# Kernel tuning notes

Hardware: AMD Instinct MI355X
Metric: run time of the kernel (lower is better)

## Reference

```python
import jax, jax.numpy as jnp
import numpy as np

N, E, E_LG, H, KGE, NUM_GRAPHS, N_ITER = 100000, 500000, 1000000, 128, 128, 1024, 2
EPS = 1e-5

def _prelu(x, a):
    return jnp.where(x >= 0, x, a * x)

def _seg_mean(vals, idx, num):
    s = jax.ops.segment_sum(vals, idx, num_segments=num)
    c = jax.ops.segment_sum(jnp.ones((vals.shape[0],), vals.dtype), idx, num_segments=num)
    return s / jnp.maximum(c, 1.0)[:, None]

def setup_inputs() -> dict:
    key = jax.random.key(0)
    ks = jax.random.split(key, 16)
    sc = 1.0 / np.sqrt(H)
    inp = {
        "x": jax.random.normal(ks[0], (N, H), jnp.float32),
        "edge_attr": jax.random.normal(ks[1], (E, H), jnp.float32),
        "edge_index": jax.random.randint(ks[2], (2, E), 0, N),
        "batch": jnp.sort(jax.random.randint(ks[3], (N,), 0, NUM_GRAPHS)),
        "line_graph_edge_index": jax.random.randint(ks[4], (2, E_LG), 0, E),
        # edge_update_net: Linear + PReLU + BatchNorm1d (eval mode)
        "W1": jax.random.normal(ks[5], (H, H), jnp.float32) * sc,
        "b1": jnp.zeros((H,), jnp.float32),
        "a1": jnp.full((1,), 0.25, jnp.float32),
        "bn_gamma": jnp.ones((H,), jnp.float32),
        "bn_beta": jnp.zeros((H,), jnp.float32),
        "bn_mean": jnp.zeros((H,), jnp.float32),
        "bn_var": jnp.ones((H,), jnp.float32),
        # GRU (single layer, single step)
        "w_ih": jax.random.normal(ks[6], (3 * H, H), jnp.float32) * sc,
        "w_hh": jax.random.normal(ks[7], (3 * H, H), jnp.float32) * sc,
        "b_ih": jnp.zeros((3 * H,), jnp.float32),
        "b_hh": jnp.zeros((3 * H,), jnp.float32),
        # DynamicAttention net
        "Wa1": jax.random.normal(ks[8], (H // 2, H), jnp.float32) * sc,
        "ba1": jnp.zeros((H // 2,), jnp.float32),
        "a2": jnp.full((1,), 0.25, jnp.float32),
        "Wa2": jax.random.normal(ks[9], (1, H // 2), jnp.float32) * (1.0 / np.sqrt(H // 2)),
        "ba2": jnp.zeros((1,), jnp.float32),
        # readout
        "Wr": jax.random.normal(ks[10], (KGE, H), jnp.float32) * sc,
        "br": jnp.zeros((KGE,), jnp.float32),
    }
    return inp

def reference(x, edge_attr, W1, b1, a1, bn_gamma, bn_beta, bn_mean, bn_var,
              w_ih, w_hh, b_ih, b_hh, Wa1, ba1, a2, Wa2, ba2, Wr, br,
              edge_index, batch, line_graph_edge_index):
    src, dst = edge_index[0], edge_index[1]
    l_src, l_dst = line_graph_edge_index[0], line_graph_edge_index[1]
    h = x  # GRU hidden state [N, H]
    for _ in range(N_ITER):
        # edge-to-edge message passing (node_to_edge_proj is Identity here)
        fused = edge_attr + (x[src] + x[dst]) * 0.5  # [E, H]
        agg = _seg_mean(fused[l_src], l_dst, E)      # scatter-mean over line graph
        upd = _prelu(agg @ W1.T + b1, a1)
        upd = (upd - bn_mean) * jax.lax.rsqrt(bn_var + EPS) * bn_gamma + bn_beta
        fused = fused + upd
        node_updates = _seg_mean(fused, dst, N)      # [N, H]
        # single GRU step
        gi = node_updates @ w_ih.T + b_ih
        gh = h @ w_hh.T + b_hh
        gi_r, gi_z, gi_n = jnp.split(gi, 3, axis=-1)
        gh_r, gh_z, gh_n = jnp.split(gh, 3, axis=-1)
        r = jax.nn.sigmoid(gi_r + gh_r)
        z = jax.nn.sigmoid(gi_z + gh_z)
        n = jnp.tanh(gi_n + r * gh_n)
        h = (1.0 - z) * n + z * h
        x = h
    # dynamic attention: per-graph scalar gate
    graph_repr = _seg_mean(x, batch, NUM_GRAPHS)     # [G, H]
    attn = jax.nn.sigmoid(_prelu(graph_repr @ Wa1.T + ba1, a2) @ Wa2.T + ba2)  # [G, 1]
    attended = x * attn[batch]
    graph_emb = jax.ops.segment_sum(attended, batch, num_segments=NUM_GRAPHS)
    graph_emb = graph_emb @ Wr.T + br
    return (x, graph_emb)
```

## Files before the change

### kernel.cpp

```cpp
#include <hip/hip_runtime.h>
#include <stdint.h>

#define H 128
#define G_NUM 1024
#define BN_EPS 1e-5f
#define IDXCAP 512

typedef unsigned int uint;
typedef unsigned short ushort;
typedef unsigned char uchar;
typedef __attribute__((ext_vector_type(8))) __bf16 bf16x8;
typedef __attribute__((ext_vector_type(8))) ushort ushort8;
typedef __attribute__((ext_vector_type(4))) float f32x4;
typedef __attribute__((ext_vector_type(2))) float f32x2;

__device__ __forceinline__ float b2f(ushort u){ return __uint_as_float(((uint)u) << 16); }
__device__ __forceinline__ ushort f2b(float f){
    uint u = __float_as_uint(f);
    u += 0x7FFFu + ((u >> 16) & 1u);
    return (ushort)(u >> 16);
}
__device__ __forceinline__ float ldf(const void* p, size_t i, int bf){
    return bf ? b2f(((const ushort*)p)[i]) : ((const float*)p)[i];
}
__device__ __forceinline__ int swz(int r, int byte_in_row){
    return (r * 256 + byte_in_row) ^ ((r & 7) << 4);
}

#define GBODY(SRC, sA, sB) do{ \
    uint4 wA_ = *(const uint4*)((SRC) + (size_t)(sA) * H + ch16 * 8); \
    uint4 wB_ = *(const uint4*)((SRC) + (size_t)(sB) * H + ch16 * 8); \
    uint wa_[4] = {wA_.x, wA_.y, wA_.z, wA_.w}; \
    uint wb_[4] = {wB_.x, wB_.y, wB_.z, wB_.w}; \
    _Pragma("unroll") \
    for (int k2 = 0; k2 < 4; k2++){ \
        f32x2 va_, vb_; \
        va_.x = __uint_as_float(wa_[k2] << 16); va_.y = __uint_as_float(wa_[k2] & 0xFFFF0000u); \
        vb_.x = __uint_as_float(wb_[k2] << 16); vb_.y = __uint_as_float(wb_[k2] & 0xFFFF0000u); \
        accA[k2] += va_; accB[k2] += vb_; \
    } }while(0)

__global__ void k_setup_small(const uint* __restrict__ gamma_bits,
                              const void* b1, const void* a1, const void* gam, const void* bet,
                              const void* mean, const void* var, const void* bih, const void* bhh,
                              float* __restrict__ ep, float* __restrict__ bi, float* __restrict__ bh,
                              int* __restrict__ flag, ushort* __restrict__ fz1, ushort* __restrict__ fz2,
                              size_t zoff, int* __restrict__ lg_off, int E, int ELG,
                              int* __restrict__ nd_off, int N, int Etot){
    __shared__ int bfs;
    int t = threadIdx.x;
    if (t == 0){
        int f = (gamma_bits[0] == 0x3F803F80u) ? 1 : 0;
        *flag = f; bfs = f;
        lg_off[E] = ELG;
        nd_off[N] = Etot;
    }
    __syncthreads();
    int bf = bfs;
    bi[t] = ldf(bih, t, bf);
    bh[t] = ldf(bhh, t, bf);
    if (t < 128){
        ep[t]       = ldf(b1, t, bf);
        ep[128 + t] = rsqrtf(ldf(var, t, bf) + BN_EPS) * ldf(gam, t, bf);
        ep[256 + t] = ldf(mean, t, bf);
        ep[384 + t] = ldf(bet, t, bf);
        fz1[zoff + t] = 0; fz2[zoff + t] = 0;
    }
    if (t == 0) ep[512] = ldf(a1, 0, bf);
}

__global__ __launch_bounds__(256) void k_count_nd(const int* __restrict__ ei, int* __restrict__ cnt, int E){
    int t = blockIdx.x * 256 + threadIdx.x;
    if (t < E) atomicAdd(&cnt[ei[E + t]], 1);
}
__global__ __launch_bounds__(256) void k_fill_nd(const int* __restrict__ ei, const int* __restrict__ off,
                                                 int* __restrict__ cur, int* __restrict__ list, int E){
    int t = blockIdx.x * 256 + threadIdx.x;
    if (t >= E) return;
    int k = ei[E + t];
    int pos = atomicAdd(&cur[k], 1);
    list[off[k] + pos] = t;
}
__global__ __launch_bounds__(256) void k_rank(const int* __restrict__ nd_list, int* __restrict__ rank,
                                              int2* __restrict__ eis, int* __restrict__ e_orig,
                                              const int* __restrict__ ei, int E){
    int j = blockIdx.x * 256 + threadIdx.x;
    if (j >= E) return;
    int e = nd_list[j];
    rank[e] = j;
    eis[j] = make_int2(ei[e], ei[E + e]);
    e_orig[j] = e;
}
__global__ __launch_bounds__(256) void k_count_lg(const int* __restrict__ lgi, const int* __restrict__ rank,
                                                  int* __restrict__ cnt, int ELG){
    int t = blockIdx.x * 256 + threadIdx.x;
    if (t < ELG) atomicAdd(&cnt[rank[lgi[ELG + t]]], 1);
}
__global__ __launch_bounds__(256) void k_fill_lg(const int* __restrict__ lgi, const int* __restrict__ rank,
                                                 const int* __restrict__ off, int* __restrict__ cur,
                                                 int* __restrict__ list, int ELG){
    int t = blockIdx.x * 256 + threadIdx.x;
    if (t >= ELG) return;
    int k = rank[lgi[ELG + t]];
    int pos = atomicAdd(&cur[k], 1);
    list[off[k] + pos] = rank[lgi[t]];
}
__global__ __launch_bounds__(256) void k_scan_reduce(const int* __restrict__ cnt, int* __restrict__ bsum, int n){
    int base = blockIdx.x * 1024;
    int s = 0;
    for (int i = threadIdx.x; i < 1024; i += 256){ int idx = base + i; s += (idx < n) ? cnt[idx] : 0; }
    __shared__ int r[256];
    r[threadIdx.x] = s; __syncthreads();
    for (int o = 128; o > 0; o >>= 1){ if (threadIdx.x < o) r[threadIdx.x] += r[threadIdx.x + o]; __syncthreads(); }
    if (threadIdx.x == 0) bsum[blockIdx.x] = r[0];
}
__global__ __launch_bounds__(256) void k_scan_mid(int* __restrict__ bsum, int nb){
    __shared__ int ts[256];
    int tid = threadIdx.x;
    int loc[4]; int s = 0;
    #pragma unroll
    for (int j = 0; j < 4; j++){
        int idx = tid * 4 + j;
        loc[j] = s;
        s += (idx < nb) ? bsum[idx] : 0;
    }
    ts[tid] = s; __syncthreads();
    for (int o = 1; o < 256; o <<= 1){
        int v = (tid >= o) ? ts[tid - o] : 0;
        __syncthreads();
        ts[tid] += v;
        __syncthreads();
    }
    int texcl = ts[tid] - s;
    #pragma unroll
    for (int j = 0; j < 4; j++){
        int idx = tid * 4 + j;
        if (idx < nb) bsum[idx] = texcl + loc[j];
    }
}
__global__ __launch_bounds__(256) void k_scan_final(const int* __restrict__ cnt, const int* __restrict__ bsum,
                                                    int* __restrict__ off, int n){
    __shared__ int ts[256];
    int base = blockIdx.x * 1024;
    int tid = threadIdx.x;
    int loc[4]; int s = 0;
    #pragma unroll
    for (int j = 0; j < 4; j++){
        int idx = base + tid * 4 + j;
        loc[j] = s;
        s += (idx < n) ? cnt[idx] : 0;
    }
    ts[tid] = s; __syncthreads();
    for (int o = 1; o < 256; o <<= 1){
        int v = (tid >= o) ? ts[tid - o] : 0;
        __syncthreads();
        ts[tid] += v;
        __syncthreads();
    }
    int texcl = ts[tid] - s + bsum[blockIdx.x];
    #pragma unroll
    for (int j = 0; j < 4; j++){
        int idx = base + tid * 4 + j;
        if (idx < n) off[idx] = texcl + loc[j];
    }
}
__global__ __launch_bounds__(256) void k_sortperm(const int* __restrict__ off, uchar* __restrict__ perm, int NK){
    int t = blockIdx.x * 256 + threadIdx.x;
    int wave = t >> 6;
    int l = t & 63;
    int l5 = l & 31;
    int r0 = wave * 32;
    if (r0 >= NK) return;
    int r = r0 + l5;
    int deg = off[r + 1] - off[r];
    int key = (deg << 5) | l5;
    #pragma unroll
    for (int k = 2; k <= 32; k <<= 1){
        #pragma unroll
        for (int j = k >> 1; j > 0; j >>= 1){
            int other = __shfl_xor(key, j);
            bool dir = ((l5 & k) == 0);
            bool lower = ((l5 & j) == 0);
            int mn = min(key, other), mx = max(key, other);
            key = (dir == lower) ? mn : mx;
        }
    }
    if (l < 32) perm[r0 + l5] = (uchar)(key & 31);
}
__global__ __launch_bounds__(256) void k_cvt_bf(const void* __restrict__ in, ushort* __restrict__ out,
                                                int n, const int* __restrict__ flag){
    int t = blockIdx.x * 256 + threadIdx.x;
    if (t >= n) return;
    if (*flag) out[t] = ((const ushort*)in)[t];
    else       out[t] = f2b(((const float*)in)[t]);
}
__global__ __launch_bounds__(256) void k_wcvt(const void* __restrict__ W1, const void* __restrict__ wih,
                                              const void* __restrict__ whh, const void* __restrict__ Wr,
                                              ushort* __restrict__ W1bf, ushort* __restrict__ wihbf,
                                              ushort* __restrict__ whhbf, float* __restrict__ WrT,
                                              const int* __restrict__ flag){
    int t = blockIdx.x * 256 + threadIdx.x;
    int bf = *flag;
    if (t < 16384) W1bf[t] = bf ? ((const ushort*)W1)[t] : f2b(((const float*)W1)[t]);
    else if (t < 65536){ int i = t - 16384; wihbf[i] = bf ? ((const ushort*)wih)[i] : f2b(((const float*)wih)[i]); }
    else if (t < 114688){ int i = t - 65536; whhbf[i] = bf ? ((const ushort*)whh)[i] : f2b(((const float*)whh)[i]); }
    else if (t < 131072){ int i = t - 114688; int r = i >> 7, c = i & 127; WrT[c * 128 + r] = ldf(Wr, i, bf); }
}

__global__ __launch_bounds__(256) void k_fused(const void* __restrict__ ea, const ushort* __restrict__ hb,
                                               const int2* __restrict__ eis, const int* __restrict__ e_orig,
                                               ushort* __restrict__ fused, int E, const int* __restrict__ flag){
    int t = blockIdx.x * 256 + threadIdx.x;
    if (t >= E * 16) return;
    int bf = *flag;
    int j = t >> 4, ch = (t & 15) * 8;
    int2 sd = eis[j];
    int e = e_orig[j];
    size_t src = (size_t)e * H + ch;
    ushort8 hs = *(const ushort8*)(hb + (size_t)sd.x * H + ch);
    ushort8 hd = *(const ushort8*)(hb + (size_t)sd.y * H + ch);
    float av[8];
    if (bf){
        ushort8 a = *(const ushort8*)((const ushort*)ea + src);
        #pragma unroll
        for (int k = 0; k < 8; k++) av[k] = b2f(a[k]);
    } else {
        float4 a0 = *(const float4*)((const float*)ea + src);
        float4 a1 = *(const float4*)((const float*)ea + src + 4);
        av[0] = a0.x; av[1] = a0.y; av[2] = a0.z; av[3] = a0.w;
        av[4] = a1.x; av[5] = a1.y; av[6] = a1.z; av[7] = a1.w;
    }
    ushort8 o;
    #pragma unroll
    for (int k = 0; k < 8; k++) o[k] = f2b(av[k] + 0.5f * (b2f(hs[k]) + b2f(hd[k])));
    *(ushort8*)(fused + (size_t)j * H + ch) = o;
}

__global__ __launch_bounds__(256) void k_agg_gemm(const ushort* __restrict__ fused,
                                                  const int* __restrict__ lg_off, const int* __restrict__ list,
                                                  const uchar* __restrict__ perm,
                                                  const ushort* __restrict__ W1bf, const float* __restrict__ ep,
                                                  ushort* __restrict__ fused2, int E, int LMAX){
    __shared__ __attribute__((aligned(16))) char As[32 * 256];
    __shared__ int idxL[IDXCAP];
    __shared__ int offL[33];
    int tid = threadIdx.x, wid = tid >> 6, lane = tid & 63;
    int r0 = blockIdx.x * 32;
    if (tid < 33) offL[tid] = lg_off[r0 + tid];
    __syncthreads();
    int seg_s = offL[0], seglen = offL[32] - seg_s;
    bool staged = (seglen <= IDXCAP);
    if (staged){ for (int j = tid; j < seglen; j += 256) idxL[j] = list[seg_s + j]; }
    __syncthreads();
    int l16 = lane >> 4, ch16 = lane & 15;
    int rA = wid * 8 + l16, rB = rA + 4;
    int plA = perm[r0 + rA], plB = perm[r0 + rB];
    int baseA = offL[plA], degA = offL[plA + 1] - baseA;
    int baseB = offL[plB], degB = offL[plB + 1] - baseB;
    int dm = max(degA, degB);
    #pragma unroll
    for (int o = 32; o > 0; o >>= 1) dm = max(dm, __shfl_xor(dm, o));
    f32x2 accA[4] = {}, accB[4] = {};
    if (staged){
        int relA = baseA - seg_s, relB = baseB - seg_s;
        #pragma unroll 2
        for (int i = 0; i < dm; i++){
            int liA = min(relA + i, seglen - 1);
            int liB = min(relB + i, seglen - 1);
            int sA = idxL[liA];
            int sB = idxL[liB];
            sA = (i < degA) ? sA : E;
            sB = (i < degB) ? sB : E;
            GBODY(fused, sA, sB);
        }
    } else {
        #pragma unroll 2
        for (int i = 0; i < dm; i++){
            int liA = baseA + i; liA = (liA < LMAX) ? liA : (LMAX - 1);
            int liB = baseB + i; liB = (liB < LMAX) ? liB : (LMAX - 1);
            int sA = list[liA];
            int sB = list[liB];
            sA = (i < degA) ? sA : E;
            sB = (i < degB) ? sB : E;
            GBODY(fused, sA, sB);
        }
    }
    float invA = 1.f / fmaxf((float)degA, 1.f);
    float invB = 1.f / fmaxf((float)degB, 1.f);
    ushort8 oA, oB;
    #pragma unroll
    for (int k2 = 0; k2 < 4; k2++){
        oA[2 * k2] = f2b(accA[k2].x * invA); oA[2 * k2 + 1] = f2b(accA[k2].y * invA);
        oB[2 * k2] = f2b(accB[k2].x * invB); oB[2 * k2 + 1] = f2b(accB[k2].y * invB);
    }
    *(ushort8*)(As + swz(plA, ch16 * 16)) = oA;
    *(ushort8*)(As + swz(plB, ch16 * 16)) = oB;
    __syncthreads();
    int lrow = lane & 15, lhi = lane >> 4;
    f32x4 acc[2][2] = {};
    #pragma unroll
    for (int ks = 0; ks < 4; ks++){
        bf16x8 afr[2];
        #pragma unroll
        for (int rt = 0; rt < 2; rt++)
            afr[rt] = *(const bf16x8*)(As + swz(rt * 16 + lrow, ks * 64 + lhi * 16));
        #pragma unroll
        for (int cc = 0; cc < 2; cc++){
            int c = (2 * wid + cc) * 16 + lrow;
            bf16x8 bfr = *(const bf16x8*)(W1bf + (size_t)c * H + ks * 32 + lhi * 8);
            #pragma unroll
            for (int rt = 0; rt < 2; rt++)
                acc[cc][rt] = __builtin_amdgcn_mfma_f32_16x16x32_bf16(afr[rt], bfr, acc[cc][rt], 0, 0, 0);
        }
    }
    __syncthreads();
    float aa = ep[512];
    #pragma unroll
    for (int cc = 0; cc < 2; cc++){
        int c = (2 * wid + cc) * 16 + lrow;
        float bb = ep[c], sc = ep[128 + c], mb = ep[256 + c], be = ep[384 + c];
        #pragma unroll
        for (int rt = 0; rt < 2; rt++)
            #pragma unroll
            for (int rg = 0; rg < 4; rg++){
                int r = rt * 16 + lhi * 4 + rg;
                float u = acc[cc][rt][rg] + bb;
                u = (u >= 0.f) ? u : aa * u;
                u = (u - mb) * sc + be;
                *(ushort*)(As + swz(r, c * 2)) = f2b(u);
            }
    }
    __syncthreads();
    #pragma unroll
    for (int q = 0; q < 2; q++){
        int r = (q == 0) ? rA : rB;
        size_t gbase = (size_t)(r0 + r) * H + ch16 * 8;
        ushort8 f = *(const ushort8*)(fused + gbase);
        ushort8 u = *(const ushort8*)(As + swz(r, ch16 * 16));
        ushort8 o;
        #pragma unroll
        for (int j = 0; j < 8; j++) o[j] = f2b(b2f(f[j]) + b2f(u[j]));
        *(ushort8*)(fused2 + gbase) = o;
    }
}

__global__ __launch_bounds__(256) void k_nodeagg(const ushort* __restrict__ fused2,
                                                 const int* __restrict__ nd_off, const uchar* __restrict__ perm,
                                                 ushort* __restrict__ NU, int N, int EZ){
    __shared__ int offL[33];
    int tid = threadIdx.x, wid = tid >> 6, lane = tid & 63;
    int r0 = blockIdx.x * 32;
    if (tid < 33) offL[tid] = nd_off[r0 + tid];
    __syncthreads();
    int l16 = lane >> 4, ch16 = lane & 15;
    int rA = wid * 8 + l16, rB = rA + 4;
    int plA = perm[r0 + rA], plB = perm[r0 + rB];
    int baseA = offL[plA], degA = offL[plA + 1] - baseA;
    int baseB = offL[plB], degB = offL[plB + 1] - baseB;
    int dm = max(degA, degB);
    #pragma unroll
    for (int o = 32; o > 0; o >>= 1) dm = max(dm, __shfl_xor(dm, o));
    f32x2 accA[4] = {}, accB[4] = {};
    #pragma unroll 2
    for (int i = 0; i < dm; i++){
        int sA = (i < degA) ? (baseA + i) : EZ;
        int sB = (i < degB) ? (baseB + i) : EZ;
        GBODY(fused2, sA, sB);
    }
    float invA = 1.f / fmaxf((float)degA, 1.f);
    float invB = 1.f / fmaxf((float)degB, 1.f);
    ushort8 oA, oB;
    #pragma unroll
    for (int k2 = 0; k2 < 4; k2++){
        oA[2 * k2] = f2b(accA[k2].x * invA); oA[2 * k2 + 1] = f2b(accA[k2].y * invA);
        oB[2 * k2] = f2b(accB[k2].x * invB); oB[2 * k2 + 1] = f2b(accB[k2].y * invB);
    }
    *(ushort8*)(NU + (size_t)(r0 + plA) * H + ch16 * 8) = oA;
    *(ushort8*)(NU + (size_t)(r0 + plB) * H + ch16 * 8) = oB;
}

__global__ __launch_bounds__(256) void k_gru_dense(const ushort* __restrict__ NU_g,
                                                   ushort* __restrict__ hb,
                                                   const ushort* __restrict__ wihbf, const ushort* __restrict__ whhbf,
                                                   const float* __restrict__ bi, const float* __restrict__ bh, int N){
    __shared__ __attribute__((aligned(16))) char NUs[32 * 256];
    __shared__ __attribute__((aligned(16))) char HHs[32 * 256];
    int tid = threadIdx.x, wid = tid >> 6, lane = tid & 63;
    int r0 = blockIdx.x * 32;
    int l16 = lane >> 4, ch16 = lane & 15;
    int rA = wid * 8 + l16, rB = rA + 4;
    *(ushort8*)(NUs + swz(rA, ch16 * 16)) = *(const ushort8*)(NU_g + (size_t)(r0 + rA) * H + ch16 * 8);
    *(ushort8*)(NUs + swz(rB, ch16 * 16)) = *(const ushort8*)(NU_g + (size_t)(r0 + rB) * H + ch16 * 8);
    *(ushort8*)(HHs + swz(rA, ch16 * 16)) = *(const ushort8*)(hb + (size_t)(r0 + rA) * H + ch16 * 8);
    *(ushort8*)(HHs + swz(rB, ch16 * 16)) = *(const ushort8*)(hb + (size_t)(r0 + rB) * H + ch16 * 8);
    __syncthreads();
    int lrow = lane & 15, lhi = lane >> 4;
    ushort hnew[2][2][4];
    #pragma unroll 1
    for (int b = 0; b < 2; b++){
        f32x4 aR[2] = {}, aZ[2] = {}, aIn[2] = {}, aHn[2] = {};
        #pragma unroll
        for (int ks = 0; ks < 4; ks++){
            bf16x8 fN[2], fH[2];
            #pragma unroll
            for (int rt = 0; rt < 2; rt++){
                int addr = swz(rt * 16 + lrow, ks * 64 + lhi * 16);
                fN[rt] = *(const bf16x8*)(NUs + addr);
                fH[rt] = *(const bf16x8*)(HHs + addr);
            }
            int cb = (wid + 4 * b) * 16 + lrow;
            size_t wofs = ks * 32 + lhi * 8;
            bf16x8 wIr = *(const bf16x8*)(wihbf + (size_t)(cb) * H + wofs);
            bf16x8 wHr = *(const bf16x8*)(whhbf + (size_t)(cb) * H + wofs);
            bf16x8 wIz = *(const bf16x8*)(wihbf + (size_t)(128 + cb) * H + wofs);
            bf16x8 wHz = *(const bf16x8*)(whhbf + (size_t)(128 + cb) * H + wofs);
            bf16x8 wIn_ = *(const bf16x8*)(wihbf + (size_t)(256 + cb) * H + wofs);
            bf16x8 wHn_ = *(const bf16x8*)(whhbf + (size_t)(256 + cb) * H + wofs);
            #pragma unroll
            for (int rt = 0; rt < 2; rt++){
                aR[rt]  = __builtin_amdgcn_mfma_f32_16x16x32_bf16(fN[rt], wIr,  aR[rt], 0, 0, 0);
                aR[rt]  = __builtin_amdgcn_mfma_f32_16x16x32_bf16(fH[rt], wHr,  aR[rt], 0, 0, 0);
                aZ[rt]  = __builtin_amdgcn_mfma_f32_16x16x32_bf16(fN[rt], wIz,  aZ[rt], 0, 0, 0);
                aZ[rt]  = __builtin_amdgcn_mfma_f32_16x16x32_bf16(fH[rt], wHz,  aZ[rt], 0, 0, 0);
                aIn[rt] = __builtin_amdgcn_mfma_f32_16x16x32_bf16(fN[rt], wIn_, aIn[rt], 0, 0, 0);
                aHn[rt] = __builtin_amdgcn_mfma_f32_16x16x32_bf16(fH[rt], wHn_, aHn[rt], 0, 0, 0);
            }
        }
        int c = (wid + 4 * b) * 16 + lrow;
        float brz = bi[c] + bh[c];
        float bzz = bi[128 + c] + bh[128 + c];
        float bin = bi[256 + c], bhn = bh[256 + c];
        #pragma unroll
        for (int rt = 0; rt < 2; rt++)
            #pragma unroll
            for (int rg = 0; rg < 4; rg++){
                int r = rt * 16 + lhi * 4 + rg;
                float rv = 1.f / (1.f + __expf(-(aR[rt][rg] + brz)));
                float zv = 1.f / (1.f + __expf(-(aZ[rt][rg] + bzz)));
                float nv = tanhf(aIn[rt][rg] + bin + rv * (aHn[rt][rg] + bhn));
                float hold = b2f(*(const ushort*)(HHs + swz(r, c * 2)));
                hnew[b][rt][rg] = f2b((1.f - zv) * nv + zv * hold);
            }
    }
    __syncthreads();
    #pragma unroll
    for (int b = 0; b < 2; b++){
        int c = (wid + 4 * b) * 16 + lrow;
        #pragma unroll
        for (int rt = 0; rt < 2; rt++)
            #pragma unroll
            for (int rg = 0; rg < 4; rg++){
                int r = rt * 16 + lhi * 4 + rg;
                *(ushort*)(NUs + swz(r, c * 2)) = hnew[b][rt][rg];
            }
    }
    __syncthreads();
    *(ushort8*)(hb + (size_t)(r0 + rA) * H + ch16 * 8) = *(const ushort8*)(NUs + swz(rA, ch16 * 16));
    *(ushort8*)(hb + (size_t)(r0 + rB) * H + ch16 * 8) = *(const ushort8*)(NUs + swz(rB, ch16 * 16));
}

__global__ __launch_bounds__(256) void k_gbounds(const int* __restrict__ batch, int* __restrict__ gs, int N, int G){
    int g = blockIdx.x * 256 + threadIdx.x;
    if (g > G) return;
    int lo = 0, hi = N;
    while (lo < hi){ int mid = (lo + hi) >> 1; if (batch[mid] < g) lo = mid + 1; else hi = mid; }
    gs[g] = lo;
}
__global__ __launch_bounds__(256) void k_graph_sum(const ushort* __restrict__ hb, const int* __restrict__ gs,
                                                   float* __restrict__ gsum, void* __restrict__ out,
                                                   const int* __restrict__ flag){
    int g = blockIdx.x, c = threadIdx.x & 127, half = threadIdx.x >> 7;
    int bf = *flag;
    int s = gs[g], e = gs[g + 1];
    float acc0 = 0.f, acc1 = 0.f;
    int r = s + half;
    for (; r + 2 < e; r += 4){
        ushort u0 = hb[(size_t)r * H + c];
        ushort u1 = hb[(size_t)(r + 2) * H + c];
        float v0 = b2f(u0), v1 = b2f(u1);
        acc0 += v0; acc1 += v1;
        if (bf){ ((ushort*)out)[(size_t)r * H + c] = u0; ((ushort*)out)[(size_t)(r + 2) * H + c] = u1; }
        else   { ((float*) out)[(size_t)r * H + c] = v0; ((float*) out)[(size_t)(r + 2) * H + c] = v1; }
    }
    for (; r < e; r += 2){
        ushort u0 = hb[(size_t)r * H + c];
        float v0 = b2f(u0);
        acc0 += v0;
        if (bf) ((ushort*)out)[(size_t)r * H + c] = u0;
        else    ((float*) out)[(size_t)r * H + c] = v0;
    }
    __shared__ float tmp[128];
    if (half == 1) tmp[c] = acc0 + acc1;
    __syncthreads();
    if (half == 0) gsum[(size_t)g * H + c] = acc0 + acc1 + tmp[c];
}
__global__ void k_attn(const float* __restrict__ gsum, const int* __restrict__ gs,
                       const void* __restrict__ Wa1, const void* __restrict__ ba1,
                       const void* __restrict__ a2, const void* __restrict__ Wa2,
                       const void* __restrict__ ba2, float* __restrict__ attn, const int* __restrict__ flag){
    int g = blockIdx.x;
    int j = threadIdx.x;
    int bf = *flag;
    float inv = 1.0f / fmaxf((float)(gs[g + 1] - gs[g]), 1.0f);
    __shared__ float R[H];
    for (int i = j; i < H; i += 64) R[i] = gsum[(size_t)g * H + i] * inv;
    __syncthreads();
    float t = 0.f;
    for (int k = 0; k < H; k++) t += R[k] * ldf(Wa1, (size_t)j * H + k, bf);
    t += ldf(ba1, j, bf);
    float al = ldf(a2, 0, bf);
    t = (t >= 0.f) ? t : al * t;
    float p = t * ldf(Wa2, j, bf);
    #pragma unroll
    for (int o = 32; o > 0; o >>= 1) p += __shfl_down(p, o);
    if (j == 0) attn[g] = 1.f / (1.f + __expf(-(p + ldf(ba2, 0, bf))));
}
__global__ __launch_bounds__(256) void k_graph_gemm(const float* __restrict__ gsum, const float* __restrict__ attn,
                                                    const float* __restrict__ WrT,
                                                    const void* __restrict__ br, void* __restrict__ out,
                                                    size_t obase, const int* __restrict__ flag){
    __shared__ float A[8 * H];
    int bf = *flag;
    int r0 = blockIdx.x * 8;
    for (int i = threadIdx.x; i < 8 * H; i += 256){
        int r = i >> 7;
        A[i] = gsum[(size_t)(r0 + r) * H + (i & 127)] * attn[r0 + r];
    }
    __syncthreads();
    int c = threadIdx.x & 127;
    int rr = (threadIdx.x >> 7) * 4;
    float acc[4] = {0, 0, 0, 0};
    for (int k = 0; k < H; k++){
        float w = WrT[k * H + c];
        #pragma unroll
        for (int j = 0; j < 4; j++) acc[j] += A[(rr + j) * H + k] * w;
    }
    float bb = ldf(br, c, bf);
    for (int j = 0; j < 4; j++){
        size_t idx = obase + (size_t)(r0 + rr + j) * H + c;
        float v = acc[j] + bb;
        if (bf) ((ushort*)out)[idx] = f2b(v);
        else    ((float*) out)[idx] = v;
    }
}

extern "C" void kernel_launch(void* const* d_in, const int* in_sizes, int n_in,
                              void* d_out, int out_size, void* d_ws, size_t ws_size,
                              hipStream_t stream)
{
    const void* x    = d_in[0];
    const void* ea   = d_in[1];
    const int*  ei   = (const int*)d_in[2];
    const int*  batch= (const int*)d_in[3];
    const int*  lgi  = (const int*)d_in[4];
    const void* W1   = d_in[5];
    const void* b1   = d_in[6];
    const void* a1   = d_in[7];
    const void* bng  = d_in[8];
    const void* bnb  = d_in[9];
    const void* bnm  = d_in[10];
    const void* bnv  = d_in[11];
    const void* wih  = d_in[12];
    const void* whh  = d_in[13];
    const void* bih  = d_in[14];
    const void* bhh  = d_in[15];
    const void* Wa1  = d_in[16];
    const void* ba1  = d_in[17];
    const void* a2   = d_in[18];
    const void* Wa2  = d_in[19];
    const void* ba2  = d_in[20];
    const void* Wr   = d_in[21];
    const void* br   = d_in[22];

    const int N   = in_sizes[0] / H;
    const int E   = in_sizes[1] / H;
    const int ELG = in_sizes[4] / 2;
    const int G   = G_NUM;
    const int nb_lg = (E + 1023) / 1024;
    const int nb_nd = (N + 1023) / 1024;

    char* ws = (char*)d_ws;
    size_t off = 0;
    auto alloc = [&](size_t b) -> void* { void* p = ws + off; off += (b + 255) & ~(size_t)255; return p; };
    int*    flag    = (int*)   alloc(256);
    ushort* hb      = (ushort*)alloc((size_t)N * H * 2);
    ushort* NUb     = (ushort*)alloc((size_t)N * H * 2);
    ushort* fused   = (ushort*)alloc((size_t)(E + 1) * H * 2);
    ushort* fused2  = (ushort*)alloc((size_t)(E + 1) * H * 2);
    int*    zreg    = (int*)   alloc((size_t)(2 * E + 2 * N) * 4);
    int*    lg_cnt  = zreg;
    int*    lg_cur  = zreg + E;
    int*    nd_cnt  = zreg + 2 * E;
    int*    nd_cur  = zreg + 2 * E + N;
    int*    lg_off  = (int*)   alloc((size_t)(E + 1) * 4);
    int*    nd_off  = (int*)   alloc((size_t)(N + 1) * 4);
    int*    lg_list = (int*)   alloc((size_t)ELG * 4);
    int*    nd_list = (int*)   alloc((size_t)E * 4);
    int*    rank    = (int*)   alloc((size_t)E * 4);
    int2*   eis     = (int2*)  alloc((size_t)E * 8);
    int*    e_orig  = (int*)   alloc((size_t)E * 4);
    uchar*  perm_lg = (uchar*) alloc((size_t)(E + 32));
    uchar*  perm_nd = (uchar*) alloc((size_t)(N + 32));
    int*    bsumA   = (int*)   alloc((size_t)(nb_lg + 8) * 4);
    int*    bsumB   = (int*)   alloc((size_t)(nb_nd + 8) * 4);
    int*    gs      = (int*)   alloc((size_t)(G + 1) * 4);
    ushort* W1bf    = (ushort*)alloc(128 * 128 * 2);
    ushort* wihbf   = (ushort*)alloc(384 * 128 * 2);
    ushort* whhbf   = (ushort*)alloc(384 * 128 * 2);
    float*  ep      = (float*) alloc(513 * 4);
    float*  bi      = (float*) alloc(384 * 4);
    float*  bh      = (float*) alloc(384 * 4);
    float*  WrT     = (float*) alloc(128 * 128 * 4);
    float*  gsum    = (float*) alloc((size_t)G * H * 4);
    float*  attn    = (float*) alloc((size_t)G * 4);

    k_setup_small<<<1, 384, 0, stream>>>((const uint*)bng, b1, a1, bng, bnb, bnm, bnv, bih, bhh,
                                         ep, bi, bh, flag, fused, fused2, (size_t)E * H,
                                         lg_off, E, ELG, nd_off, N, E);

    hipMemsetAsync(zreg, 0, (size_t)(2 * E + 2 * N) * 4, stream);
    k_count_nd<<<(E + 255) / 256, 256, 0, stream>>>(ei, nd_cnt, E);
    k_scan_reduce<<<nb_nd, 256, 0, stream>>>(nd_cnt, bsumB, N);
    k_scan_mid<<<1, 256, 0, stream>>>(bsumB, nb_nd);
    k_scan_final<<<nb_nd, 256, 0, stream>>>(nd_cnt, bsumB, nd_off, N);
    k_fill_nd<<<(E + 255) / 256, 256, 0, stream>>>(ei, nd_off, nd_cur, nd_list, E);
    k_rank<<<(E + 255) / 256, 256, 0, stream>>>(nd_list, rank, eis, e_orig, ei, E);
    k_count_lg<<<(ELG + 255) / 256, 256, 0, stream>>>(lgi, rank, lg_cnt, ELG);
    k_scan_reduce<<<nb_lg, 256, 0, stream>>>(lg_cnt, bsumA, E);
    k_scan_mid<<<1, 256, 0, stream>>>(bsumA, nb_lg);
    k_scan_final<<<nb_lg, 256, 0, stream>>>(lg_cnt, bsumA, lg_off, E);
    k_fill_lg<<<(ELG + 255) / 256, 256, 0, stream>>>(lgi, rank, lg_off, lg_cur, lg_list, ELG);
    k_sortperm<<<(E / 32 * 64 + 255) / 256, 256, 0, stream>>>(lg_off, perm_lg, E);
    k_sortperm<<<(N / 32 * 64 + 255) / 256, 256, 0, stream>>>(nd_off, perm_nd, N);

    k_wcvt<<<(131072 + 255) / 256, 256, 0, stream>>>(W1, wih, whh, Wr, W1bf, wihbf, whhbf, WrT, flag);

    k_cvt_bf<<<(N * H + 255) / 256, 256, 0, stream>>>(x, hb, N * H, flag);

    for (int it = 0; it < 2; it++){
        k_fused<<<(E * 16 + 255) / 256, 256, 0, stream>>>(ea, hb, eis, e_orig, fused, E, flag);
        k_agg_gemm<<<(E + 31) / 32, 256, 0, stream>>>(fused, lg_off, lg_list, perm_lg, W1bf, ep, fused2, E, ELG);
        k_nodeagg<<<(N + 31) / 32, 256, 0, stream>>>(fused2, nd_off, perm_nd, NUb, N, E);
        k_gru_dense<<<(N + 31) / 32, 256, 0, stream>>>(NUb, hb, wihbf, whhbf, bi, bh, N);
    }

    k_gbounds<<<(G + 256) / 256, 256, 0, stream>>>(batch, gs, N, G);
    k_graph_sum<<<G, 256, 0, stream>>>(hb, gs, gsum, d_out, flag);
    k_attn<<<G, 64, 0, stream>>>(gsum, gs, Wa1, ba1, a2, Wa2, ba2, attn, flag);
    k_graph_gemm<<<G / 8, 256, 0, stream>>>(gsum, attn, WrT, br, d_out, (size_t)N * H, flag);
}
```

Before: 964.5 us.

## Fuse node aggregation into GRU kernel and merge rank into fill pass

The per-node mean aggregation now writes its result straight into shared memory inside the GRU kernel, so the bf16 node-update buffer no longer goes to global memory and one launch per iteration disappears. Separately, the edge fill kernel computes rank, the sorted endpoint pairs and the original edge ids directly, which removes the nd_list buffer and the k_rank launch. The cost is a larger fused kernel whose gather loop and MFMA GEMM share registers and LDS, which may lower occupancy.

```diff
diff --git a/kernel.cpp b/kernel.cpp
--- a/kernel.cpp
+++ b/kernel.cpp
@@ -74,22 +74,16 @@
     if (t < E) atomicAdd(&cnt[ei[E + t]], 1);
 }
 __global__ __launch_bounds__(256) void k_fill_nd(const int* __restrict__ ei, const int* __restrict__ off,
-                                                 int* __restrict__ cur, int* __restrict__ list, int E){
+                                                 int* __restrict__ cur, int* __restrict__ rank,
+                                                 int2* __restrict__ eis, int* __restrict__ e_orig, int E){
     int t = blockIdx.x * 256 + threadIdx.x;
     if (t >= E) return;
     int k = ei[E + t];
     int pos = atomicAdd(&cur[k], 1);
-    list[off[k] + pos] = t;
-}
-__global__ __launch_bounds__(256) void k_rank(const int* __restrict__ nd_list, int* __restrict__ rank,
-                                              int2* __restrict__ eis, int* __restrict__ e_orig,
-                                              const int* __restrict__ ei, int E){
-    int j = blockIdx.x * 256 + threadIdx.x;
-    if (j >= E) return;
-    int e = nd_list[j];
-    rank[e] = j;
-    eis[j] = make_int2(ei[e], ei[E + e]);
-    e_orig[j] = e;
+    int j = off[k] + pos;
+    rank[t] = j;
+    eis[j] = make_int2(ei[t], ei[E + t]);
+    e_orig[j] = t;
 }
 __global__ __launch_bounds__(256) void k_count_lg(const int* __restrict__ lgi, const int* __restrict__ rank,
                                                   int* __restrict__ cnt, int ELG){
@@ -344,16 +338,23 @@
     }
 }
 
-__global__ __launch_bounds__(256) void k_nodeagg(const ushort* __restrict__ fused2,
-                                                 const int* __restrict__ nd_off, const uchar* __restrict__ perm,
-                                                 ushort* __restrict__ NU, int N, int EZ){
+__global__ __launch_bounds__(256) void k_gru_fused(const ushort* __restrict__ fused2,
+                                                   const int* __restrict__ nd_off, const uchar* __restrict__ perm,
+                                                   ushort* __restrict__ hb,
+                                                   const ushort* __restrict__ wihbf, const ushort* __restrict__ whhbf,
+                                                   const float* __restrict__ bi, const float* __restrict__ bh,
+                                                   int N, int EZ){
+    __shared__ __attribute__((aligned(16))) char NUs[32 * 256];
+    __shared__ __attribute__((aligned(16))) char HHs[32 * 256];
     __shared__ int offL[33];
     int tid = threadIdx.x, wid = tid >> 6, lane = tid & 63;
     int r0 = blockIdx.x * 32;
     if (tid < 33) offL[tid] = nd_off[r0 + tid];
-    __syncthreads();
     int l16 = lane >> 4, ch16 = lane & 15;
     int rA = wid * 8 + l16, rB = rA + 4;
+    *(ushort8*)(HHs + swz(rA, ch16 * 16)) = *(const ushort8*)(hb + (size_t)(r0 + rA) * H + ch16 * 8);
+    *(ushort8*)(HHs + swz(rB, ch16 * 16)) = *(const ushort8*)(hb + (size_t)(r0 + rB) * H + ch16 * 8);
+    __syncthreads();
     int plA = perm[r0 + rA], plB = perm[r0 + rB];
     int baseA = offL[plA], degA = offL[plA + 1] - baseA;
     int baseB = offL[plB], degB = offL[plB + 1] - baseB;
@@ -375,24 +376,8 @@
         oA[2 * k2] = f2b(accA[k2].x * invA); oA[2 * k2 + 1] = f2b(accA[k2].y * invA);
         oB[2 * k2] = f2b(accB[k2].x * invB); oB[2 * k2 + 1] = f2b(accB[k2].y * invB);
     }
-    *(ushort8*)(NU + (size_t)(r0 + plA) * H + ch16 * 8) = oA;
-    *(ushort8*)(NU + (size_t)(r0 + plB) * H + ch16 * 8) = oB;
-}
-
-__global__ __launch_bounds__(256) void k_gru_dense(const ushort* __restrict__ NU_g,
-                                                   ushort* __restrict__ hb,
-                                                   const ushort* __restrict__ wihbf, const ushort* __restrict__ whhbf,
-                                                   const float* __restrict__ bi, const float* __restrict__ bh, int N){
-    __shared__ __attribute__((aligned(16))) char NUs[32 * 256];
-    __shared__ __attribute__((aligned(16))) char HHs[32 * 256];
-    int tid = threadIdx.x, wid = tid >> 6, lane = tid & 63;
-    int r0 = blockIdx.x * 32;
-    int l16 = lane >> 4, ch16 = lane & 15;
-    int rA = wid * 8 + l16, rB = rA + 4;
-    *(ushort8*)(NUs + swz(rA, ch16 * 16)) = *(const ushort8*)(NU_g + (size_t)(r0 + rA) * H + ch16 * 8);
-    *(ushort8*)(NUs + swz(rB, ch16 * 16)) = *(const ushort8*)(NU_g + (size_t)(r0 + rB) * H + ch16 * 8);
-    *(ushort8*)(HHs + swz(rA, ch16 * 16)) = *(const ushort8*)(hb + (size_t)(r0 + rA) * H + ch16 * 8);
-    *(ushort8*)(HHs + swz(rB, ch16 * 16)) = *(const ushort8*)(hb + (size_t)(r0 + rB) * H + ch16 * 8);
+    *(ushort8*)(NUs + swz(plA, ch16 * 16)) = oA;
+    *(ushort8*)(NUs + swz(plB, ch16 * 16)) = oB;
     __syncthreads();
     int lrow = lane & 15, lhi = lane >> 4;
     ushort hnew[2][2][4];
@@ -584,7 +569,6 @@
     auto alloc = [&](size_t b) -> void* { void* p = ws + off; off += (b + 255) & ~(size_t)255; return p; };
     int*    flag    = (int*)   alloc(256);
     ushort* hb      = (ushort*)alloc((size_t)N * H * 2);
-    ushort* NUb     = (ushort*)alloc((size_t)N * H * 2);
     ushort* fused   = (ushort*)alloc((size_t)(E + 1) * H * 2);
     ushort* fused2  = (ushort*)alloc((size_t)(E + 1) * H * 2);
     int*    zreg    = (int*)   alloc((size_t)(2 * E + 2 * N) * 4);
@@ -595,7 +579,6 @@
     int*    lg_off  = (int*)   alloc((size_t)(E + 1) * 4);
     int*    nd_off  = (int*)   alloc((size_t)(N + 1) * 4);
     int*    lg_list = (int*)   alloc((size_t)ELG * 4);
-    int*    nd_list = (int*)   alloc((size_t)E * 4);
     int*    rank    = (int*)   alloc((size_t)E * 4);
     int2*   eis     = (int2*)  alloc((size_t)E * 8);
     int*    e_orig  = (int*)   alloc((size_t)E * 4);
@@ -623,8 +606,7 @@
     k_scan_reduce<<<nb_nd, 256, 0, stream>>>(nd_cnt, bsumB, N);
     k_scan_mid<<<1, 256, 0, stream>>>(bsumB, nb_nd);
     k_scan_final<<<nb_nd, 256, 0, stream>>>(nd_cnt, bsumB, nd_off, N);
-    k_fill_nd<<<(E + 255) / 256, 256, 0, stream>>>(ei, nd_off, nd_cur, nd_list, E);
-    k_rank<<<(E + 255) / 256, 256, 0, stream>>>(nd_list, rank, eis, e_orig, ei, E);
+    k_fill_nd<<<(E + 255) / 256, 256, 0, stream>>>(ei, nd_off, nd_cur, rank, eis, e_orig, E);
     k_count_lg<<<(ELG + 255) / 256, 256, 0, stream>>>(lgi, rank, lg_cnt, ELG);
     k_scan_reduce<<<nb_lg, 256, 0, stream>>>(lg_cnt, bsumA, E);
     k_scan_mid<<<1, 256, 0, stream>>>(bsumA, nb_lg);
@@ -640,8 +622,7 @@
     for (int it = 0; it < 2; it++){
         k_fused<<<(E * 16 + 255) / 256, 256, 0, stream>>>(ea, hb, eis, e_orig, fused, E, flag);
         k_agg_gemm<<<(E + 31) / 32, 256, 0, stream>>>(fused, lg_off, lg_list, perm_lg, W1bf, ep, fused2, E, ELG);
-        k_nodeagg<<<(N + 31) / 32, 256, 0, stream>>>(fused2, nd_off, perm_nd, NUb, N, E);
-        k_gru_dense<<<(N + 31) / 32, 256, 0, stream>>>(NUb, hb, wihbf, whhbf, bi, bh, N);
+        k_gru_fused<<<(N + 31) / 32, 256, 0, stream>>>(fused2, nd_off, perm_nd, hb, wihbf, whhbf, bi, bh, N, E);
     }
 
     k_gbounds<<<(G + 256) / 256, 256, 0, stream>>>(batch, gs, N, G);
```

After: 972.1 us. No clear change (+0.8%).
